# Kernel tuning notes

Hardware: AMD Instinct MI355X
Metric: run time of the kernel (lower is better)

## Reference

```python
import jax, jax.numpy as jnp
import numpy as np

D_MODEL = 1024
NUM_HEADS = 16
D_K = D_MODEL // NUM_HEADS


def setup_inputs() -> dict:
    key = jax.random.key(0)
    ks = jax.random.split(key, 11)
    B, S = 2, 2048
    s = 1.0 / np.sqrt(D_MODEL)
    inp = {
        'Q': jax.random.normal(ks[0], (B, S, D_MODEL), jnp.float32),
        'K': jax.random.normal(ks[1], (B, S, D_MODEL), jnp.float32),
        'V': jax.random.normal(ks[2], (B, S, D_MODEL), jnp.float32),
        'Wq': jax.random.normal(ks[3], (D_MODEL, D_MODEL), jnp.float32) * s,
        'bq': jnp.zeros((D_MODEL,), jnp.float32),
        'Wk': jax.random.normal(ks[4], (D_MODEL, D_MODEL), jnp.float32) * s,
        'bk': jnp.zeros((D_MODEL,), jnp.float32),
        'Wv': jax.random.normal(ks[5], (D_MODEL, D_MODEL), jnp.float32) * s,
        'bv': jnp.zeros((D_MODEL,), jnp.float32),
        'Wo': jax.random.normal(ks[6], (D_MODEL, D_MODEL), jnp.float32) * s,
        'bo': jnp.zeros((D_MODEL,), jnp.float32),
    }
    return inp


def _split_heads(x, B):
    # [B, S, D] -> [B, H, S, d_k]
    return x.reshape(B, -1, NUM_HEADS, D_K).transpose(0, 2, 1, 3)


def reference(Q, K, V, Wq, bq, Wk, bk, Wv, bv, Wo, bo):
    B, S, _ = Q.shape
    q = _split_heads(Q @ Wq.T + bq, B)  # [B,H,S,dk]
    k = _split_heads(K @ Wk.T + bk, B)
    v = _split_heads(V @ Wv.T + bv, B)
    scale = 1.0 / jnp.sqrt(jnp.asarray(D_K, q.dtype))
    scores = jnp.einsum('bhqd,bhkd->bhqk', q, k) * scale  # full [B,H,S,S] (naive)
    attn = jax.nn.softmax(scores, axis=-1)
    ctx = jnp.einsum('bhqk,bhkd->bhqd', attn, v)
    ctx = ctx.transpose(0, 2, 1, 3).reshape(B, S, D_MODEL)
    out = ctx @ Wo.T + bo  # dropout in eval mode = identity
    return out
```

## Files before the change

kernel.cpp:

```cpp
#include <hip/hip_runtime.h>
#include <hip/hip_bf16.h>


typedef __attribute__((ext_vector_type(8))) short short8;
typedef __attribute__((ext_vector_type(4))) float f32x4;
typedef __attribute__((ext_vector_type(4))) unsigned short us4;

static constexpr int D_MODEL = 1024;
static constexpr int NHEAD   = 16;
static constexpr int DK      = 64;
static constexpr int SEQ     = 2048;
static constexpr int BATCH   = 2;
static constexpr int MTOT    = BATCH * SEQ;

static constexpr float QSCL = 0.125f * 1.44269504088896340736f;

#define DEVINL __device__ __forceinline__

DEVINL unsigned short f2bf(float f) {
    __hip_bfloat16 h = __float2bfloat16(f);
    return *reinterpret_cast<unsigned short*>(&h);
}

__global__ __launch_bounds__(256) void cast_f32_bf16(
    const float* __restrict__ s0, const float* __restrict__ s1,
    const float* __restrict__ s2, const float* __restrict__ s3,
    unsigned short* __restrict__ d0, unsigned short* __restrict__ d1,
    unsigned short* __restrict__ d2, unsigned short* __restrict__ d3,
    int n)
{
    const float* s; unsigned short* d;
    switch (blockIdx.y) {
        case 0:  s = s0; d = d0; break;
        case 1:  s = s1; d = d1; break;
        case 2:  s = s2; d = d2; break;
        default: s = s3; d = d3; break;
    }
    int i = (blockIdx.x * 256 + threadIdx.x) * 8;
    if (i + 8 > n) return;
    float4 v0 = *reinterpret_cast<const float4*>(s + i);
    float4 v1 = *reinterpret_cast<const float4*>(s + i + 4);
    union { unsigned short u[8]; short8 v; } o;
    o.u[0] = f2bf(v0.x); o.u[1] = f2bf(v0.y); o.u[2] = f2bf(v0.z); o.u[3] = f2bf(v0.w);
    o.u[4] = f2bf(v1.x); o.u[5] = f2bf(v1.y); o.u[6] = f2bf(v1.z); o.u[7] = f2bf(v1.w);
    *reinterpret_cast<short8*>(d + i) = o.v;
}

template<int MODE>
DEVINL void gemm_core(const unsigned short* __restrict__ A,
                      const unsigned short* __restrict__ W,
                      const float* __restrict__ bias,
                      void* __restrict__ outp,
                      int m0, int n0, float oscale,
                      unsigned short* a_lds, unsigned short* b_lds)
{
    constexpr int K = 1024;
    const int tid  = threadIdx.x;
    const int wave = tid >> 6, lane = tid & 63;
    const int wrow = (wave >> 1) * 64, wcol = (wave & 1) * 64;
    const int fr = lane & 15, fg = lane >> 4;

    f32x4 acc[4][4];
    #pragma unroll
    for (int i = 0; i < 4; ++i)
        #pragma unroll
        for (int j = 0; j < 4; ++j)
            acc[i][j] = (f32x4){0.f, 0.f, 0.f, 0.f};

    const int c0 = tid, c1 = tid + 256;
    const unsigned short* gA0 = A + (size_t)(m0 + (c0 >> 2)) * K + (c0 & 3) * 8;
    const unsigned short* gA1 = A + (size_t)(m0 + (c1 >> 2)) * K + (c1 & 3) * 8;
    const unsigned short* gB0 = W + (size_t)(n0 + (c0 >> 2)) * K + (c0 & 3) * 8;
    const unsigned short* gB1 = W + (size_t)(n0 + (c1 >> 2)) * K + (c1 & 3) * 8;
    char* aLb = (char*)a_lds + wave * 1024;
    char* bLb = (char*)b_lds + wave * 1024;

    auto stage = [&](int buf, int kt) {
        const int bo = buf * 8192;
        __builtin_amdgcn_global_load_lds(gA0 + kt * 32, aLb + bo,        16, 0, 0);
        __builtin_amdgcn_global_load_lds(gA1 + kt * 32, aLb + bo + 4096, 16, 0, 0);
        __builtin_amdgcn_global_load_lds(gB0 + kt * 32, bLb + bo,        16, 0, 0);
        __builtin_amdgcn_global_load_lds(gB1 + kt * 32, bLb + bo + 4096, 16, 0, 0);
    };

    stage(0, 0);
    __syncthreads();
    int cur = 0;

    for (int kt = 0; kt < K / 32; ++kt) {
        if (kt + 1 < K / 32) stage(cur ^ 1, kt + 1);

        const unsigned short* aF = a_lds + cur * 4096 + (wrow + fr) * 32 + fg * 8;
        const unsigned short* bF = b_lds + cur * 4096 + (wcol + fr) * 32 + fg * 8;
        short8 af[4], bf[4];
        #pragma unroll
        for (int mt = 0; mt < 4; ++mt)
            af[mt] = *reinterpret_cast<const short8*>(aF + mt * 16 * 32);
        #pragma unroll
        for (int nt = 0; nt < 4; ++nt)
            bf[nt] = *reinterpret_cast<const short8*>(bF + nt * 16 * 32);
        __builtin_amdgcn_s_setprio(1);
        #pragma unroll
        for (int mt = 0; mt < 4; ++mt)
            #pragma unroll
            for (int nt = 0; nt < 4; ++nt)
                acc[mt][nt] = __builtin_amdgcn_mfma_f32_16x16x32_bf16(
                    af[mt], bf[nt], acc[mt][nt], 0, 0, 0);
        __builtin_amdgcn_s_setprio(0);

        __syncthreads();
        cur ^= 1;
    }

    #pragma unroll
    for (int mt = 0; mt < 4; ++mt) {
        #pragma unroll
        for (int nt = 0; nt < 4; ++nt) {
            f32x4 v = acc[mt][nt];
            const int n = n0 + wcol + nt * 16 + fr;
            const float bi = bias[n];
            if constexpr (MODE == 2) {
                #pragma unroll
                for (int r = 0; r < 4; ++r) {
                    const int m = m0 + wrow + mt * 16 + fg * 4 + r;
                    ((float*)outp)[(size_t)m * D_MODEL + n] = (v[r] + bi) * oscale;
                }
            } else if constexpr (MODE == 0) {
                #pragma unroll
                for (int r = 0; r < 4; ++r) {
                    const int m = m0 + wrow + mt * 16 + fg * 4 + r;
                    const int b = m >> 11, s = m & 2047;
                    const int h = n >> 6,  d = n & 63;
                    ((unsigned short*)outp)[((size_t)(b * NHEAD + h) * SEQ + s) * DK + d]
                        = f2bf((v[r] + bi) * oscale);
                }
            } else {
                const int sbase = m0 + wrow + mt * 16 + fg * 4;
                const int b = sbase >> 11, s = sbase & 2047;
                const int h = n >> 6, d = n & 63;
                us4 pk;
                #pragma unroll
                for (int r = 0; r < 4; ++r)
                    pk[r] = f2bf((v[r] + bi) * oscale);
                *reinterpret_cast<us4*>(
                    (unsigned short*)outp
                    + ((size_t)(b * NHEAD + h) * DK + d) * SEQ + s) = pk;
            }
        }
    }
}

__global__ __launch_bounds__(256) void qkv_gemm(
    const unsigned short* __restrict__ Qb, const unsigned short* __restrict__ Kb,
    const unsigned short* __restrict__ Vb,
    const unsigned short* __restrict__ Wq, const unsigned short* __restrict__ Wk,
    const unsigned short* __restrict__ Wv,
    const float* __restrict__ bq, const float* __restrict__ bk,
    const float* __restrict__ bv,
    unsigned short* __restrict__ qh, unsigned short* __restrict__ kh,
    unsigned short* __restrict__ vT)
{
    __shared__ unsigned short a_lds[2 * 128 * 32];
    __shared__ unsigned short b_lds[2 * 128 * 32];
    const int sel = blockIdx.y >> 3;
    const int n0  = (blockIdx.y & 7) * 128;
    const int m0  = blockIdx.x * 128;
    if (sel == 0)      gemm_core<0>(Qb, Wq, bq, qh, m0, n0, QSCL, a_lds, b_lds);
    else if (sel == 1) gemm_core<0>(Kb, Wk, bk, kh, m0, n0, 1.0f, a_lds, b_lds);
    else               gemm_core<1>(Vb, Wv, bv, vT, m0, n0, 1.0f, a_lds, b_lds);
}

__global__ __launch_bounds__(256) void oproj_gemm(
    const unsigned short* __restrict__ ctx, const unsigned short* __restrict__ Wo,
    const float* __restrict__ bo, float* __restrict__ out)
{
    __shared__ unsigned short a_lds[2 * 128 * 32];
    __shared__ unsigned short b_lds[2 * 128 * 32];
    gemm_core<2>(ctx, Wo, bo, out, blockIdx.x * 128, blockIdx.y * 128, 1.0f,
                 a_lds, b_lds);
}

__global__ __launch_bounds__(256) void attn_fwd(
    const unsigned short* __restrict__ qh,
    const unsigned short* __restrict__ kh,
    const unsigned short* __restrict__ vT,
    unsigned short* __restrict__ ctx)
{
    __shared__ unsigned short k_lds[2][64 * 64];
    __shared__ unsigned short v_lds[2][64 * 64];
    __shared__ unsigned short p_lds[4][16 * 64];

    const int tid  = threadIdx.x;
    const int wave = tid >> 6, lane = tid & 63;
    const int fr = lane & 15, fg = lane >> 4;
    const int swz = (fr & 7) << 4;
    const int h = blockIdx.y, b = blockIdx.z;
    const int q0 = blockIdx.x * 64 + wave * 16;

    const size_t headoff = (size_t)(b * NHEAD + h) * SEQ * DK;
    const unsigned short* qbase = qh + headoff;
    const unsigned short* kbase = kh + headoff;
    const unsigned short* vbase = vT + headoff;

    short8 qf[2];
    #pragma unroll
    for (int ks = 0; ks < 2; ++ks)
        qf[ks] = *reinterpret_cast<const short8*>(
            qbase + (size_t)(q0 + fr) * DK + ks * 32 + fg * 8);

    const int c0 = tid, c1 = 256 + tid;
    const int r0 = c0 >> 3, s0i = (c0 & 7) ^ (r0 & 7);
    const int r1 = c1 >> 3, s1i = (c1 & 7) ^ (r1 & 7);
    const unsigned short* gk0 = kbase + (size_t)r0 * DK + s0i * 8;
    const unsigned short* gk1 = kbase + (size_t)r1 * DK + s1i * 8;
    const unsigned short* gv0 = vbase + (size_t)r0 * SEQ + s0i * 8;
    const unsigned short* gv1 = vbase + (size_t)r1 * SEQ + s1i * 8;

    auto stage = [&](int buf, int kv0) {
        char* kb = (char*)k_lds[buf] + wave * 1024;
        char* vb = (char*)v_lds[buf] + wave * 1024;
        __builtin_amdgcn_global_load_lds(gk0 + (size_t)kv0 * DK, kb,        16, 0, 0);
        __builtin_amdgcn_global_load_lds(gk1 + (size_t)kv0 * DK, kb + 4096, 16, 0, 0);
        __builtin_amdgcn_global_load_lds(gv0 + kv0,              vb,        16, 0, 0);
        __builtin_amdgcn_global_load_lds(gv1 + kv0,              vb + 4096, 16, 0, 0);
    };

    f32x4 oacc[4];
    #pragma unroll
    for (int i = 0; i < 4; ++i) oacc[i] = (f32x4){0.f, 0.f, 0.f, 0.f};
    float mrun[4], lpart[4];
    #pragma unroll
    for (int r = 0; r < 4; ++r) { mrun[r] = -1e30f; lpart[r] = 0.f; }

    constexpr float THR = 8.0f;

    char* pwr = (char*)p_lds[wave];
    const char* prd = (const char*)p_lds[wave] + fr * 128;

    stage(0, 0);
    __syncthreads();
    int cur = 0;

    for (int kt = 0; kt < SEQ / 64; ++kt) {
        if (kt + 1 < SEQ / 64) stage(cur ^ 1, (kt + 1) * 64);

        const char* kl = (const char*)k_lds[cur];
        const char* vl = (const char*)v_lds[cur];

        f32x4 sacc[4];
        #pragma unroll
        for (int i = 0; i < 4; ++i) sacc[i] = (f32x4){0.f, 0.f, 0.f, 0.f};
        __builtin_amdgcn_s_setprio(1);
        #pragma unroll
        for (int ks = 0; ks < 2; ++ks) {
            #pragma unroll
            for (int nt = 0; nt < 4; ++nt) {
                const int krow = nt * 16 + fr;
                short8 kf = *reinterpret_cast<const short8*>(
                    kl + krow * 128 + ((ks * 64 + fg * 16) ^ swz));
                sacc[nt] = __builtin_amdgcn_mfma_f32_16x16x32_bf16(
                    qf[ks], kf, sacc[nt], 0, 0, 0);
            }
        }
        __builtin_amdgcn_s_setprio(0);

        float lmax[4];
        bool need = false;
        #pragma unroll
        for (int r = 0; r < 4; ++r) {
            lmax[r] = fmaxf(fmaxf(sacc[0][r], sacc[1][r]),
                            fmaxf(sacc[2][r], sacc[3][r]));
            need |= (lmax[r] > mrun[r] + THR);
        }
        if (__any(need)) {
            #pragma unroll
            for (int r = 0; r < 4; ++r) {
                float mx = fmaxf(lmax[r], mrun[r]);
                mx = fmaxf(mx, __shfl_xor(mx, 1));
                mx = fmaxf(mx, __shfl_xor(mx, 2));
                mx = fmaxf(mx, __shfl_xor(mx, 4));
                mx = fmaxf(mx, __shfl_xor(mx, 8));
                const float alpha = __builtin_amdgcn_exp2f(mrun[r] - mx);
                mrun[r] = mx;
                lpart[r] *= alpha;
                #pragma unroll
                for (int ntd = 0; ntd < 4; ++ntd)
                    oacc[ntd][r] *= alpha;
            }
        }

        #pragma unroll
        for (int r = 0; r < 4; ++r) {
            float rs = 0.f;
            #pragma unroll
            for (int nt = 0; nt < 4; ++nt) {
                const float p = __builtin_amdgcn_exp2f(sacc[nt][r] - mrun[r]);
                sacc[nt][r] = p;
                rs += p;
            }
            lpart[r] += rs;
        }

        #pragma unroll
        for (int nt = 0; nt < 4; ++nt)
            #pragma unroll
            for (int r = 0; r < 4; ++r) {
                const int qrow = fg * 4 + r;
                *(unsigned short*)(pwr + qrow * 128
                    + ((nt * 32 + fr * 2) ^ ((qrow & 7) << 4)))
                    = f2bf(sacc[nt][r]);
            }

        #pragma unroll
        for (int ks = 0; ks < 2; ++ks) {
            short8 pf = *reinterpret_cast<const short8*>(
                prd + ((ks * 64 + fg * 16) ^ swz));
            __builtin_amdgcn_s_setprio(1);
            #pragma unroll
            for (int ntd = 0; ntd < 4; ++ntd) {
                const int vrow = ntd * 16 + fr;
                short8 vf = *reinterpret_cast<const short8*>(
                    vl + vrow * 128 + ((ks * 64 + fg * 16) ^ swz));
                oacc[ntd] = __builtin_amdgcn_mfma_f32_16x16x32_bf16(
                    pf, vf, oacc[ntd], 0, 0, 0);
            }
            __builtin_amdgcn_s_setprio(0);
        }

        __syncthreads();
        cur ^= 1;
    }

    float inv[4];
    #pragma unroll
    for (int r = 0; r < 4; ++r) {
        float s = lpart[r];
        s += __shfl_xor(s, 1);
        s += __shfl_xor(s, 2);
        s += __shfl_xor(s, 4);
        s += __shfl_xor(s, 8);
        inv[r] = 1.f / s;
    }
    #pragma unroll
    for (int ntd = 0; ntd < 4; ++ntd)
        #pragma unroll
        for (int r = 0; r < 4; ++r) {
            const int qg = q0 + fg * 4 + r;
            const size_t off = ((size_t)(b * SEQ + qg)) * D_MODEL
                             + h * DK + ntd * 16 + fr;
            ctx[off] = f2bf(oacc[ntd][r] * inv[r]);
        }
}

extern "C" void kernel_launch(void* const* d_in, const int* in_sizes, int n_in,
                              void* d_out, int out_size, void* d_ws, size_t ws_size,
                              hipStream_t stream)
{
    const float* Q  = (const float*)d_in[0];
    const float* K  = (const float*)d_in[1];
    const float* V  = (const float*)d_in[2];
    const float* Wq = (const float*)d_in[3];
    const float* bq = (const float*)d_in[4];
    const float* Wk = (const float*)d_in[5];
    const float* bk = (const float*)d_in[6];
    const float* Wv = (const float*)d_in[7];
    const float* bv = (const float*)d_in[8];
    const float* Wo = (const float*)d_in[9];
    const float* bo = (const float*)d_in[10];

    char* ws = (char*)d_ws;
    const size_t SZ_ACT = (size_t)MTOT * D_MODEL * 2;
    const size_t SZ_W   = (size_t)D_MODEL * D_MODEL * 2;
    unsigned short* Qb  = (unsigned short*)(ws);
    unsigned short* Kb  = (unsigned short*)(ws + SZ_ACT);
    unsigned short* Vb  = (unsigned short*)(ws + 2 * SZ_ACT);
    unsigned short* Wqb = (unsigned short*)(ws + 3 * SZ_ACT);
    unsigned short* Wkb = (unsigned short*)(ws + 3 * SZ_ACT + SZ_W);
    unsigned short* Wvb = (unsigned short*)(ws + 3 * SZ_ACT + 2 * SZ_W);
    unsigned short* Wob = (unsigned short*)(ws + 3 * SZ_ACT + 3 * SZ_W);
    unsigned short* qhd = (unsigned short*)(ws + 3 * SZ_ACT + 4 * SZ_W);
    unsigned short* khd = (unsigned short*)(ws + 4 * SZ_ACT + 4 * SZ_W);
    unsigned short* vTd = (unsigned short*)(ws + 5 * SZ_ACT + 4 * SZ_W);
    unsigned short* ctx = (unsigned short*)(ws + 6 * SZ_ACT + 4 * SZ_W);

    const int nAct = MTOT * D_MODEL;
    const int nW   = D_MODEL * D_MODEL;

    cast_f32_bf16<<<dim3(nAct / (256 * 8), 3), 256, 0, stream>>>(
        Q, K, V, nullptr, Qb, Kb, Vb, nullptr, nAct);
    cast_f32_bf16<<<dim3(nW / (256 * 8), 4), 256, 0, stream>>>(
        Wq, Wk, Wv, Wo, Wqb, Wkb, Wvb, Wob, nW);

    qkv_gemm<<<dim3(MTOT / 128, 24), 256, 0, stream>>>(
        Qb, Kb, Vb, Wqb, Wkb, Wvb, bq, bk, bv, qhd, khd, vTd);

    attn_fwd<<<dim3(SEQ / 64, NHEAD, BATCH), 256, 0, stream>>>(
        qhd, khd, vTd, ctx);

    oproj_gemm<<<dim3(MTOT / 128, D_MODEL / 128), 256, 0, stream>>>(
        ctx, Wob, bo, (float*)d_out);
}
```

Baseline: 249.3 us.

## Rework attention to 32x32 MFMA with transposed S and register-resident P

Switches the attention kernel from 16x16x32 to 32x32x16 MFMA, computing S transposed (K as A operand) so each lane owns one query row. Softmax row max and sum then need only a single cross-half shuffle, and P is repacked into B-operand fragments with lane-xor-32 shuffles instead of a round trip through LDS. Each wave now handles 32 queries and each block 128, halving K/V reloads per query but also halving the grid size. Output stores become vectorized 4-element writes.

```diff
diff --git a/kernel.cpp b/kernel.cpp
--- a/kernel.cpp
+++ b/kernel.cpp
@@ -4,6 +4,7 @@
 
 typedef __attribute__((ext_vector_type(8))) short short8;
 typedef __attribute__((ext_vector_type(4))) float f32x4;
+typedef __attribute__((ext_vector_type(16))) float f32x16;
 typedef __attribute__((ext_vector_type(4))) unsigned short us4;
 
 static constexpr int D_MODEL = 1024;
@@ -20,6 +21,13 @@
 DEVINL unsigned short f2bf(float f) {
     __hip_bfloat16 h = __float2bfloat16(f);
     return *reinterpret_cast<unsigned short*>(&h);
+}
+
+DEVINL unsigned pack2bf(float lo, float hi) {
+    union { __hip_bfloat162 h2; unsigned u; } c;
+    float2 f; f.x = lo; f.y = hi;
+    c.h2 = __float22bfloat162_rn(f);
+    return c.u;
 }
 
 __global__ __launch_bounds__(256) void cast_f32_bf16(
@@ -188,25 +196,23 @@
 {
     __shared__ unsigned short k_lds[2][64 * 64];
     __shared__ unsigned short v_lds[2][64 * 64];
-    __shared__ unsigned short p_lds[4][16 * 64];
 
     const int tid  = threadIdx.x;
     const int wave = tid >> 6, lane = tid & 63;
-    const int fr = lane & 15, fg = lane >> 4;
-    const int swz = (fr & 7) << 4;
+    const int q    = lane & 31, hi = lane >> 5;
     const int h = blockIdx.y, b = blockIdx.z;
-    const int q0 = blockIdx.x * 64 + wave * 16;
+    const int q0 = blockIdx.x * 128 + wave * 32;
 
     const size_t headoff = (size_t)(b * NHEAD + h) * SEQ * DK;
     const unsigned short* qbase = qh + headoff;
     const unsigned short* kbase = kh + headoff;
     const unsigned short* vbase = vT + headoff;
 
-    short8 qf[2];
+    short8 qf[4];
     #pragma unroll
-    for (int ks = 0; ks < 2; ++ks)
-        qf[ks] = *reinterpret_cast<const short8*>(
-            qbase + (size_t)(q0 + fr) * DK + ks * 32 + fg * 8);
+    for (int c = 0; c < 4; ++c)
+        qf[c] = *reinterpret_cast<const short8*>(
+            qbase + (size_t)(q0 + q) * DK + c * 16 + hi * 8);
 
     const int c0 = tid, c1 = 256 + tid;
     const int r0 = c0 >> 3, s0i = (c0 & 7) ^ (r0 & 7);
@@ -225,17 +231,13 @@
         __builtin_amdgcn_global_load_lds(gv1 + kv0,              vb + 4096, 16, 0, 0);
     };
 
-    f32x4 oacc[4];
+    f32x16 oacc[2];
     #pragma unroll
-    for (int i = 0; i < 4; ++i) oacc[i] = (f32x4){0.f, 0.f, 0.f, 0.f};
-    float mrun[4], lpart[4];
-    #pragma unroll
-    for (int r = 0; r < 4; ++r) { mrun[r] = -1e30f; lpart[r] = 0.f; }
-
+    for (int kd = 0; kd < 2; ++kd)
+        #pragma unroll
+        for (int r = 0; r < 16; ++r) oacc[kd][r] = 0.f;
+    float mrun = -1e30f, lpart = 0.f;
     constexpr float THR = 8.0f;
-
-    char* pwr = (char*)p_lds[wave];
-    const char* prd = (const char*)p_lds[wave] + fr * 128;
 
     stage(0, 0);
     __syncthreads();
@@ -247,108 +249,109 @@
         const char* kl = (const char*)k_lds[cur];
         const char* vl = (const char*)v_lds[cur];
 
-        f32x4 sacc[4];
-        #pragma unroll
-        for (int i = 0; i < 4; ++i) sacc[i] = (f32x4){0.f, 0.f, 0.f, 0.f};
+        f32x16 sacc[2];
+        #pragma unroll
+        for (int kb = 0; kb < 2; ++kb)
+            #pragma unroll
+            for (int r = 0; r < 16; ++r) sacc[kb][r] = 0.f;
+
         __builtin_amdgcn_s_setprio(1);
         #pragma unroll
-        for (int ks = 0; ks < 2; ++ks) {
-            #pragma unroll
-            for (int nt = 0; nt < 4; ++nt) {
-                const int krow = nt * 16 + fr;
+        for (int kb = 0; kb < 2; ++kb) {
+            const int krow = kb * 32 + q;
+            const int ksw  = (krow & 7) << 4;
+            #pragma unroll
+            for (int c = 0; c < 4; ++c) {
                 short8 kf = *reinterpret_cast<const short8*>(
-                    kl + krow * 128 + ((ks * 64 + fg * 16) ^ swz));
-                sacc[nt] = __builtin_amdgcn_mfma_f32_16x16x32_bf16(
-                    qf[ks], kf, sacc[nt], 0, 0, 0);
+                    kl + krow * 128 + ((c * 32 + hi * 16) ^ ksw));
+                sacc[kb] = __builtin_amdgcn_mfma_f32_32x32x16_bf16(
+                    kf, qf[c], sacc[kb], 0, 0, 0);
             }
         }
         __builtin_amdgcn_s_setprio(0);
 
-        float lmax[4];
-        bool need = false;
-        #pragma unroll
-        for (int r = 0; r < 4; ++r) {
-            lmax[r] = fmaxf(fmaxf(sacc[0][r], sacc[1][r]),
-                            fmaxf(sacc[2][r], sacc[3][r]));
-            need |= (lmax[r] > mrun[r] + THR);
+        float pm = sacc[0][0];
+        #pragma unroll
+        for (int r = 1; r < 16; ++r) pm = fmaxf(pm, sacc[0][r]);
+        #pragma unroll
+        for (int r = 0; r < 16; ++r) pm = fmaxf(pm, sacc[1][r]);
+        pm = fmaxf(pm, __shfl_xor(pm, 32));
+
+        if (__any(pm > mrun + THR)) {
+            const float mx = fmaxf(pm, mrun);
+            const float alpha = __builtin_amdgcn_exp2f(mrun - mx);
+            mrun = mx;
+            lpart *= alpha;
+            #pragma unroll
+            for (int kd = 0; kd < 2; ++kd)
+                #pragma unroll
+                for (int r = 0; r < 16; ++r) oacc[kd][r] *= alpha;
         }
-        if (__any(need)) {
-            #pragma unroll
-            for (int r = 0; r < 4; ++r) {
-                float mx = fmaxf(lmax[r], mrun[r]);
-                mx = fmaxf(mx, __shfl_xor(mx, 1));
-                mx = fmaxf(mx, __shfl_xor(mx, 2));
-                mx = fmaxf(mx, __shfl_xor(mx, 4));
-                mx = fmaxf(mx, __shfl_xor(mx, 8));
-                const float alpha = __builtin_amdgcn_exp2f(mrun[r] - mx);
-                mrun[r] = mx;
-                lpart[r] *= alpha;
+
+        float ps = 0.f;
+        #pragma unroll
+        for (int kb = 0; kb < 2; ++kb)
+            #pragma unroll
+            for (int r = 0; r < 16; ++r) {
+                const float p = __builtin_amdgcn_exp2f(sacc[kb][r] - mrun);
+                sacc[kb][r] = p;
+                ps += p;
+            }
+        ps += __shfl_xor(ps, 32);
+        lpart += ps;
+
+        unsigned w[2][8];
+        #pragma unroll
+        for (int kb = 0; kb < 2; ++kb)
+            #pragma unroll
+            for (int m = 0; m < 8; ++m)
+                w[kb][m] = pack2bf(sacc[kb][2 * m], sacc[kb][2 * m + 1]);
+
+        #pragma unroll
+        for (int kb = 0; kb < 2; ++kb) {
+            #pragma unroll
+            for (int kc = 0; kc < 2; ++kc) {
+                const unsigned o0 = hi ? w[kb][4 * kc + 2] : w[kb][4 * kc + 0];
+                const unsigned o1 = hi ? w[kb][4 * kc + 3] : w[kb][4 * kc + 1];
+                const unsigned sp0 = hi ? w[kb][4 * kc + 0] : w[kb][4 * kc + 2];
+                const unsigned sp1 = hi ? w[kb][4 * kc + 1] : w[kb][4 * kc + 3];
+                const unsigned e0 = (unsigned)__shfl_xor((int)sp0, 32);
+                const unsigned e1 = (unsigned)__shfl_xor((int)sp1, 32);
+                union { unsigned u[4]; short8 v; } pf;
+                pf.u[0] = hi ? e0 : o0;
+                pf.u[1] = hi ? e1 : o1;
+                pf.u[2] = hi ? o0 : e0;
+                pf.u[3] = hi ? o1 : e1;
+
+                __builtin_amdgcn_s_setprio(1);
                 #pragma unroll
-                for (int ntd = 0; ntd < 4; ++ntd)
-                    oacc[ntd][r] *= alpha;
+                for (int kd = 0; kd < 2; ++kd) {
+                    const int vrow = kd * 32 + q;
+                    const int slot = kb * 4 + kc * 2 + hi;
+                    short8 vf = *reinterpret_cast<const short8*>(
+                        vl + vrow * 128 + ((slot * 16) ^ ((vrow & 7) << 4)));
+                    oacc[kd] = __builtin_amdgcn_mfma_f32_32x32x16_bf16(
+                        vf, pf.v, oacc[kd], 0, 0, 0);
+                }
+                __builtin_amdgcn_s_setprio(0);
             }
-        }
-
-        #pragma unroll
-        for (int r = 0; r < 4; ++r) {
-            float rs = 0.f;
-            #pragma unroll
-            for (int nt = 0; nt < 4; ++nt) {
-                const float p = __builtin_amdgcn_exp2f(sacc[nt][r] - mrun[r]);
-                sacc[nt][r] = p;
-                rs += p;
-            }
-            lpart[r] += rs;
-        }
-
-        #pragma unroll
-        for (int nt = 0; nt < 4; ++nt)
-            #pragma unroll
-            for (int r = 0; r < 4; ++r) {
-                const int qrow = fg * 4 + r;
-                *(unsigned short*)(pwr + qrow * 128
-                    + ((nt * 32 + fr * 2) ^ ((qrow & 7) << 4)))
-                    = f2bf(sacc[nt][r]);
-            }
-
-        #pragma unroll
-        for (int ks = 0; ks < 2; ++ks) {
-            short8 pf = *reinterpret_cast<const short8*>(
-                prd + ((ks * 64 + fg * 16) ^ swz));
-            __builtin_amdgcn_s_setprio(1);
-            #pragma unroll
-            for (int ntd = 0; ntd < 4; ++ntd) {
-                const int vrow = ntd * 16 + fr;
-                short8 vf = *reinterpret_cast<const short8*>(
-                    vl + vrow * 128 + ((ks * 64 + fg * 16) ^ swz));
-                oacc[ntd] = __builtin_amdgcn_mfma_f32_16x16x32_bf16(
-                    pf, vf, oacc[ntd], 0, 0, 0);
-            }
-            __builtin_amdgcn_s_setprio(0);
         }
 
         __syncthreads();
         cur ^= 1;
     }
 
-    float inv[4];
+    const float inv = 1.f / lpart;
+    unsigned short* crow = ctx + ((size_t)(b * SEQ + q0 + q)) * D_MODEL + h * DK;
     #pragma unroll
-    for (int r = 0; r < 4; ++r) {
-        float s = lpart[r];
-        s += __shfl_xor(s, 1);
-        s += __shfl_xor(s, 2);
-        s += __shfl_xor(s, 4);
-        s += __shfl_xor(s, 8);
-        inv[r] = 1.f / s;
-    }
-    #pragma unroll
-    for (int ntd = 0; ntd < 4; ++ntd)
-        #pragma unroll
-        for (int r = 0; r < 4; ++r) {
-            const int qg = q0 + fg * 4 + r;
-            const size_t off = ((size_t)(b * SEQ + qg)) * D_MODEL
-                             + h * DK + ntd * 16 + fr;
-            ctx[off] = f2bf(oacc[ntd][r] * inv[r]);
+    for (int kd = 0; kd < 2; ++kd)
+        #pragma unroll
+        for (int rr = 0; rr < 4; ++rr) {
+            us4 pk;
+            #pragma unroll
+            for (int e = 0; e < 4; ++e)
+                pk[e] = f2bf(oacc[kd][rr * 4 + e] * inv);
+            *reinterpret_cast<us4*>(crow + kd * 32 + rr * 8 + hi * 4) = pk;
         }
 }
 
@@ -394,7 +397,7 @@
     qkv_gemm<<<dim3(MTOT / 128, 24), 256, 0, stream>>>(
         Qb, Kb, Vb, Wqb, Wkb, Wvb, bq, bk, bv, qhd, khd, vTd);
 
-    attn_fwd<<<dim3(SEQ / 64, NHEAD, BATCH), 256, 0, stream>>>(
+    attn_fwd<<<dim3(SEQ / 128, NHEAD, BATCH), 256, 0, stream>>>(
         qhd, khd, vTd, ctx);
 
     oproj_gemm<<<dim3(MTOT / 128, D_MODEL / 128), 256, 0, stream>>>(
```

Measured after the change: 245.9 us. About the same (-1.4%).
